# Kernel optimization log

Hardware: AMD Instinct MI355X
Metric: run time of the kernel (lower is better)

The kernel has to match this reference:

```python
import jax, jax.numpy as jnp
import numpy as np
from jax.ops import segment_sum, segment_max

N, E, B = 100000, 400000, 2048
F_NODE, F_EDGE, G_DIM = 7, 3, 10
HID, H, C, L, T = 128, 4, 32, 4, 5
EPS = 1e-5
NEG_SLOPE = 0.2

def setup_inputs():
    key = jax.random.key(0)
    ks = iter(jax.random.split(key, 64))
    def nrm(shape, fan_in):
        return jax.random.normal(next(ks), shape, jnp.float32) / np.float32(np.sqrt(fan_in))
    return {
        "x": jax.random.normal(next(ks), (N, F_NODE), jnp.float32),
        "edge_index": jax.random.randint(next(ks), (2, E), 0, N),
        "edge_attr": jax.random.normal(next(ks), (E, F_EDGE), jnp.float32),
        "batch": jnp.sort(jax.random.randint(next(ks), (N,), 0, B)),
        "global_features": jax.random.normal(next(ks), (B, G_DIM), jnp.float32),
        "node_w": nrm((F_NODE, HID), F_NODE), "node_b": jnp.zeros((HID,), jnp.float32),
        "edge_w": nrm((F_EDGE, HID), F_EDGE), "edge_b": jnp.zeros((HID,), jnp.float32),
        "gat_lin_w": nrm((L, HID, H * C), HID),
        "gat_edge_w": nrm((L, HID, H * C), HID),
        "att_src": nrm((L, H, C), C), "att_dst": nrm((L, H, C), C), "att_edge": nrm((L, H, C), C),
        "gat_bias": jnp.zeros((L, H * C), jnp.float32),
        "bn_gamma": jnp.ones((L, HID), jnp.float32), "bn_beta": jnp.zeros((L, HID), jnp.float32),
        "bn_mean": jnp.zeros((L, HID), jnp.float32), "bn_var": jnp.ones((L, HID), jnp.float32),
        "gc_w": nrm((3 * HID, HID), 3 * HID), "gc_b": jnp.zeros((HID,), jnp.float32),
        "gf1_w": nrm((G_DIM, HID // 2), G_DIM), "gf1_b": jnp.zeros((HID // 2,), jnp.float32),
        "gf2_w": nrm((HID // 2, HID // 2), HID // 2), "gf2_b": jnp.zeros((HID // 2,), jnp.float32),
        "p1_w": nrm((HID + HID // 2, HID), HID + HID // 2), "p1_b": jnp.zeros((HID,), jnp.float32),
        "p2_w": nrm((HID, HID // 2), HID), "p2_b": jnp.zeros((HID // 2,), jnp.float32),
        "p3_w": nrm((HID // 2, T), HID // 2), "p3_b": jnp.zeros((T,), jnp.float32),
    }

def _forward(x, edge_attr, global_features,
             node_w, node_b, edge_w, edge_b,
             gat_lin_w, gat_edge_w, att_src, att_dst, att_edge, gat_bias,
             bn_gamma, bn_beta, bn_mean, bn_var,
             gc_w, gc_b, gf1_w, gf1_b, gf2_w, gf2_b,
             p1_w, p1_b, p2_w, p2_b, p3_w, p3_b,
             edge_index, batch):
    n = x.shape[0]
    b = global_features.shape[0]
    src, dst = edge_index[0], edge_index[1]
    loop = jnp.arange(n)

    h = x @ node_w + node_b                       # [N, HID]
    e = edge_attr @ edge_w + edge_b               # [E, HID]

    # PyG add_self_loops with fill_value='mean': self-loop edge feature is the
    # mean of incoming edge features (0 for isolated nodes).
    deg = segment_sum(jnp.ones((src.shape[0],), h.dtype), dst, num_segments=n)
    e_loop = segment_sum(e, dst, num_segments=n) / jnp.maximum(deg, 1.0)[:, None]
    fsrc = jnp.concatenate([src, loop])
    fdst = jnp.concatenate([dst, loop])
    fe = jnp.concatenate([e, e_loop], axis=0)     # [E+N, HID]

    for i in range(L):
        h_res = h
        xh = (h @ gat_lin_w[i]).reshape(n, H, C)
        eh = (fe @ gat_edge_w[i]).reshape(-1, H, C)
        a_s = jnp.einsum('nhc,hc->nh', xh, att_src[i])
        a_d = jnp.einsum('nhc,hc->nh', xh, att_dst[i])
        a_e = jnp.einsum('ehc,hc->eh', eh, att_edge[i])
        alpha = jax.nn.leaky_relu(a_s[fsrc] + a_d[fdst] + a_e, NEG_SLOPE)  # [E+N, H]
        # segment softmax over destination neighborhoods (self loops => nonempty)
        amax = segment_max(alpha, fdst, num_segments=n)
        expa = jnp.exp(alpha - amax[fdst])
        denom = segment_sum(expa, fdst, num_segments=n)
        coef = expa / denom[fdst]
        out = segment_sum(xh[fsrc] * coef[..., None], fdst, num_segments=n)
        out = out.reshape(n, H * C) + gat_bias[i]
        # BatchNorm (eval-mode running stats)
        out = (out - bn_mean[i]) * (bn_gamma[i] / jnp.sqrt(bn_var[i] + EPS)) + bn_beta[i]
        h = jax.nn.relu(out) + h_res

    # multi-pool readout
    cnt = segment_sum(jnp.ones((n,), h.dtype), batch, num_segments=b)
    gsum = segment_sum(h, batch, num_segments=b)
    gmean = gsum / jnp.maximum(cnt, 1.0)[:, None]
    gmax = segment_max(h, batch, num_segments=b)
    gmax = jnp.where(cnt[:, None] > 0, gmax, 0.0)
    graph = jnp.concatenate([gmean, gmax, gsum], axis=1)   # [B, 3*HID]
    graph = jax.nn.relu(graph @ gc_w + gc_b)
    glob = jax.nn.relu(global_features @ gf1_w + gf1_b) @ gf2_w + gf2_b
    comb = jnp.concatenate([graph, glob], axis=1)          # [B, HID + HID//2]
    hid = jax.nn.relu(comb @ p1_w + p1_b)
    hid = jax.nn.relu(hid @ p2_w + p2_b)
    return hid @ p3_w + p3_b                               # [B, T]

def reference(x, edge_index, edge_attr, batch, global_features,
              node_w, node_b, edge_w, edge_b,
              gat_lin_w, gat_edge_w, att_src, att_dst, att_edge, gat_bias,
              bn_gamma, bn_beta, bn_mean, bn_var,
              gc_w, gc_b, gf1_w, gf1_b, gf2_w, gf2_b,
              p1_w, p1_b, p2_w, p2_b, p3_w, p3_b):
    return _forward(x, edge_attr, global_features,
                    node_w, node_b, edge_w, edge_b,
                    gat_lin_w, gat_edge_w, att_src, att_dst, att_edge, gat_bias,
                    bn_gamma, bn_beta, bn_mean, bn_var,
                    gc_w, gc_b, gf1_w, gf1_b, gf2_w, gf2_b,
                    p1_w, p1_b, p2_w, p2_b, p3_w, p3_b,
                    edge_index, batch)
```

## Files before the change

kernel.cpp:

```cpp
#include <hip/hip_runtime.h>

#define N_NODES 100000
#define N_EDGES 400000
#define N_GRAPHS 2048
#define HID 128
#define NLAYER 4
#define TOUT 5
#define EPSV 1e-5f
#define SLOPE 0.2f
#define NB 98
#define GEMM_BLOCKS 782

typedef float v4f __attribute__((ext_vector_type(4)));
typedef __bf16 v8bf __attribute__((ext_vector_type(8)));

static __device__ __forceinline__ unsigned short f2bf_bits(float f){
  unsigned u = __builtin_bit_cast(unsigned, f);
  unsigned r = u + 0x7fffu + ((u >> 16) & 1u);
  return (unsigned short)(r >> 16);
}
static __device__ __forceinline__ float bfbits2f(unsigned short s){
  unsigned u = ((unsigned)s) << 16;
  return __builtin_bit_cast(float, u);
}
static __device__ __forceinline__ float bflo(unsigned u){
  return __builtin_bit_cast(float, u << 16);
}
static __device__ __forceinline__ float bfhi(unsigned u){
  return __builtin_bit_cast(float, u & 0xffff0000u);
}
static __device__ __forceinline__ float lrelu(float v){
  return v>0.f ? v : SLOPE*v;
}


__global__ void k_setup(const float* __restrict__ gat_edge_w, const float* __restrict__ att_edge,
                        const float* __restrict__ edge_w, const float* __restrict__ edge_b,
                        const float* __restrict__ gat_bias, const float* __restrict__ gamma,
                        const float* __restrict__ beta, const float* __restrict__ mean,
                        const float* __restrict__ var, const float* __restrict__ gat_lin_w,
                        const float* __restrict__ att_src, const float* __restrict__ att_dst,
                        const float* __restrict__ x, const float* __restrict__ nw,
                        const float* __restrict__ nb, unsigned* __restrict__ h16,
                        float* __restrict__ mebuf, float* __restrict__ bnA, float* __restrict__ bnS,
                        unsigned short* __restrict__ whiE, unsigned short* __restrict__ wloE,
                        unsigned short* __restrict__ whi,
                        int* __restrict__ deg, int* __restrict__ fill){
  int bid = blockIdx.x, t = threadIdx.x;
  if(bid < 16){
    int wv = t>>6, lane = t&63;
    int o = bid*4 + wv;
    int li = (o<48)? (o&15) : (o-48);
    int f = o>>4;
    int l = li>>2, hh = li&3;
    int c = lane&31, kk = lane>>5;
    float at_c = att_edge[l*128 + hh*32 + c];
    float acc = 0.f;
    #pragma unroll 8
    for(int t2=0; t2<64; ++t2){
      int k = kk*64 + t2;
      float wk = (o<48)? edge_w[f*128+k] : edge_b[k];
      acc += wk * gat_edge_w[l*16384 + k*128 + hh*32 + c];
    }
    acc *= at_c;
    acc += __shfl_xor(acc,1); acc += __shfl_xor(acc,2); acc += __shfl_xor(acc,4);
    acc += __shfl_xor(acc,8); acc += __shfl_xor(acc,16); acc += __shfl_xor(acc,32);
    if(lane==0) mebuf[o] = acc;
  } else if(bid == 16){
    for(int i=t; i<NLAYER*HID; i+=256){
      int l_ = i>>7, pos = i&127, lane = pos>>2, j = pos&3;
      int ch = ((lane>>3)<<5) + ((lane&7)<<1) + ((j&1)<<4) + (j>>1);
      int src = l_*128 + ch;
      float A = gamma[src]*rsqrtf(var[src]+EPSV);
      bnA[i] = A;
      bnS[i] = (gat_bias[src]-mean[src])*A + beta[src];
    }
  } else if(bid <= 1040){
    int wave = t>>6, lane = t&63;
    int i = (bid-17)*8 + wave*2 + (lane>>5);
    int l_ = i>>11, rest = i&2047, kp = rest>>4, col = rest&15;
    int sub = lane&31;
    float val = 0.f;
    if(col < 8){
      int h_ = col&3, isdst = col>>2;
      int ch = ((kp>>5)<<5) + ((kp&1)<<4) + ((kp&31)>>1);
      const float* at = (isdst? att_dst : att_src);
      val = gat_lin_w[l_*16384 + ch*128 + h_*32 + sub] * at[l_*128 + h_*32 + sub];
    }
    val += __shfl_xor(val,1); val += __shfl_xor(val,2); val += __shfl_xor(val,4);
    val += __shfl_xor(val,8); val += __shfl_xor(val,16);
    if(sub == 0){
      unsigned short hi = f2bf_bits(val);
      unsigned short lo = f2bf_bits(val - bfbits2f(hi));
      int kb=kp>>5, quad=(kp>>3)&3, jj=kp&7, lane2=quad*16+col;
      int dst = ((l_*4+kb)*64 + lane2)*8 + jj;
      whiE[dst]=hi; wloE[dst]=lo;
    }
  } else if(bid <= 1296){
    int tg = (bid-1041)*256 + t;
    int base = tg>>9, off = tg&511;
    int l = base>>5, kb=(base>>3)&3, cg=base&7;
    int lane = off>>3, j = off&7;
    int quad = lane>>4, r = lane&15;
    int kp = kb*32 + quad*8 + j;
    int k = ((kp>>5)<<5) | ((kp&1)<<4) | ((kp&31)>>1);
    whi[tg] = f2bf_bits(gat_lin_w[l*16384 + k*128 + cg*16 + r]);
  } else if(bid <= 1687){
    int tg = (bid-1297)*256 + t;
    if(tg < N_NODES){ deg[tg]=0; fill[tg]=0; }
  } else {
    int node = (bid-1688)*4 + (t>>6);
    int c = t&63;
    int ch = ((c>>4)<<5) + (c&15);
    float a0 = nb[ch], a1 = nb[ch+16];
    #pragma unroll
    for(int f=0; f<7; ++f){
      float xv = x[node*7+f];
      a0 += xv*nw[f*HID+ch];
      a1 += xv*nw[f*HID+ch+16];
    }
    unsigned p = (unsigned)f2bf_bits(a0) | ((unsigned)f2bf_bits(a1)<<16);
    h16[(size_t)node*64 + c] = p;
  }
}

__global__ void k_deg(const int* __restrict__ ei, int* __restrict__ deg){
  int e = blockIdx.x*256 + threadIdx.x;
  if(e < N_EDGES) atomicAdd(&deg[ei[N_EDGES+e]], 1);
}

__global__ void k_scan1(const int* __restrict__ deg, int* __restrict__ part){
  __shared__ int s[256];
  int t=threadIdx.x; int base = blockIdx.x*1024 + t*4;
  int sum=0;
  #pragma unroll
  for(int j=0;j<4;++j){ int i=base+j; sum += (i<N_NODES)? deg[i]:0; }
  s[t]=sum; __syncthreads();
  for(int off=128; off>0; off>>=1){ if(t<off) s[t]+=s[t+off]; __syncthreads(); }
  if(t==0) part[blockIdx.x]=s[0];
}
__global__ void k_scan3(const int* __restrict__ deg, const int* __restrict__ part,
                        int* __restrict__ rowptr){
  __shared__ int s[256];
  int t=threadIdx.x, b=blockIdx.x;
  int g = 0, tot = 0;
  for(int i=0;i<NB;++i){ int v = part[i]; g += (i<b)? v : 0; tot += v; }
  if(b==0 && t==0) rowptr[N_NODES]=tot;
  int base = b*1024 + t*4;
  int v[4]; int sum=0; int pre[4];
  #pragma unroll
  for(int j=0;j<4;++j){ int i=base+j; v[j]=(i<N_NODES)?deg[i]:0; pre[j]=sum; sum+=v[j]; }
  s[t]=sum; __syncthreads();
  for(int off=1; off<256; off<<=1){
    int xv = (t>=off)? s[t-off]:0; __syncthreads();
    s[t]+=xv; __syncthreads();
  }
  int toff = (t>0)? s[t-1]:0;
  #pragma unroll
  for(int j=0;j<4;++j){ int i=base+j; if(i<N_NODES) rowptr[i]=g+toff+pre[j]; }
}

__global__ void k_gemm(const unsigned short* __restrict__ h16,
                       const unsigned short* __restrict__ whi,
                       const unsigned short* __restrict__ whiE,
                       const unsigned short* __restrict__ wloE,
                       unsigned* __restrict__ xhb, float* __restrict__ as_, float* __restrict__ ad_,
                       const int* __restrict__ ei, const float* __restrict__ ea,
                       const int* __restrict__ rowptr, int* __restrict__ fill,
                       int* __restrict__ csr_src, float* __restrict__ ea_csr){
  if(blockIdx.x >= GEMM_BLOCKS){
    int e = (blockIdx.x - GEMM_BLOCKS)*256 + threadIdx.x;
    if(e < N_EDGES){
      int dst = ei[N_EDGES+e];
      int pos = rowptr[dst] + atomicAdd(&fill[dst],1);
      csr_src[pos] = ei[e];
      v4f q = {ea[e*3], ea[e*3+1], ea[e*3+2], 0.f};
      ((v4f*)ea_csr)[pos] = q;
    }
    return;
  }
  __shared__ unsigned sxh[4][2][16*68];
  int wave = threadIdx.x>>6, lane = threadIdx.x&63;
  int base = blockIdx.x*128;
  int q = lane>>4, r = lane&15;
  int r0[2];
  r0[0] = base + wave*16;
  r0[1] = base + 64 + wave*16;
  if(r0[0] > N_NODES-16) r0[0] = N_NODES-16;
  if(r0[1] > N_NODES-16) r0[1] = N_NODES-16;
  v8bf av[2][4];
  #pragma unroll
  for(int tt=0;tt<2;++tt){
    const unsigned short* hrow = h16 + (size_t)(r0[tt] + r)*HID;
    #pragma unroll
    for(int kb=0;kb<4;++kb)
      av[tt][kb] = *(const v8bf*)(hrow + kb*32 + q*8);
  }
  v4f acc[2][8];
  #pragma unroll
  for(int cg=0;cg<8;++cg){
    v4f a0 = {0.f,0.f,0.f,0.f}, a1 = {0.f,0.f,0.f,0.f};
    #pragma unroll
    for(int kb=0;kb<4;++kb){
      v8bf bhi = *(const v8bf*)(whi + ((kb*8+cg)*64 + lane)*8);
      a0 = __builtin_amdgcn_mfma_f32_16x16x32_bf16(av[0][kb], bhi, a0, 0,0,0);
      a1 = __builtin_amdgcn_mfma_f32_16x16x32_bf16(av[1][kb], bhi, a1, 0,0,0);
    }
    acc[0][cg]=a0; acc[1][cg]=a1;
  }
  v4f acc8[2] = {{0.f,0.f,0.f,0.f},{0.f,0.f,0.f,0.f}};
  #pragma unroll
  for(int kb=0;kb<4;++kb){
    v8bf bhi = *(const v8bf*)(whiE + (kb*64 + lane)*8);
    v8bf blo = *(const v8bf*)(wloE + (kb*64 + lane)*8);
    #pragma unroll
    for(int tt=0;tt<2;++tt){
      acc8[tt] = __builtin_amdgcn_mfma_f32_16x16x32_bf16(av[tt][kb], blo, acc8[tt], 0,0,0);
      acc8[tt] = __builtin_amdgcn_mfma_f32_16x16x32_bf16(av[tt][kb], bhi, acc8[tt], 0,0,0);
    }
  }
  #pragma unroll
  for(int tt=0;tt<2;++tt){
    #pragma unroll
    for(int m=0;m<4;++m){
      #pragma unroll
      for(int reg=0;reg<4;++reg){
        unsigned pack = (unsigned)f2bf_bits(acc[tt][2*m][reg]) | ((unsigned)f2bf_bits(acc[tt][2*m+1][reg])<<16);
        sxh[wave][tt][(q*4+reg)*68 + m*16 + r] = pack;
      }
    }
  }
  __syncthreads();
  {
    int rr = lane>>4, c4 = lane&15;
    #pragma unroll
    for(int tt=0;tt<2;++tt){
      #pragma unroll
      for(int rg=0; rg<4; ++rg){
        int i = rg*4 + rr;
        uint4 v = *(const uint4*)&sxh[wave][tt][i*68 + c4*4];
        *(uint4*)(xhb + (size_t)(r0[tt] + i)*64 + c4*4) = v;
      }
    }
  }
  #pragma unroll
  for(int tt=0;tt<2;++tt){
    if(r < 4){
      #pragma unroll
      for(int reg=0;reg<4;++reg)
        as_[(size_t)(r0[tt] + q*4 + reg)*4 + r] = acc8[tt][reg];
    } else if(r < 8){
      #pragma unroll
      for(int reg=0;reg<4;++reg)
        ad_[(size_t)(r0[tt] + q*4 + reg)*4 + (r-4)] = acc8[tt][reg];
    }
  }
}

__global__ void k_aggr(const unsigned* __restrict__ xhb, const float* __restrict__ as_,
    const float* __restrict__ ad_, const float* __restrict__ ea_csr,
    const float* __restrict__ mebuf,
    const int* __restrict__ rowptr, const int* __restrict__ csr_src,
    const float* __restrict__ bnA_l, const float* __restrict__ bnS_l,
    unsigned* __restrict__ h16, int layer){
  __shared__ float lds_coef[8][16*4];
  __shared__ int   lds_src[8][16];
  int hw = threadIdx.x>>5, lh = threadIdx.x&31;
  int lane = threadIdx.x&63;
  int node = blockIdx.x*8 + hw;
  if(node >= N_NODES) return;
  int s = rowptr[node], e = rowptr[node+1];
  int deg = e - s;
  int hh2 = lh>>3;
  const uint2* xrow = (const uint2*)xhb;
  float a0,a1,a2,a3;

  if(deg <= 16){
    int eidx = lh>>2, h = lh&3;
    int li = layer*4+h;
    float mec0=mebuf[li], mec1=mebuf[16+li], mec2=mebuf[32+li], meb=mebuf[48+li];
    float ad_h = ad_[node*4+h];
    int j0 = eidx;
    float t0 = 0.f, g0 = 0.f;
    int s0 = node;
    bool v0 = (j0 < deg);
    if(v0){
      s0 = csr_src[s+j0];
      v4f qq = ((const v4f*)ea_csr)[s+j0];
      t0 = qq.x*mec0 + qq.y*mec1 + qq.z*mec2;
      g0 = lrelu(as_[s0*4+h] + ad_h + t0 + meb);
    }
    float ts, ds, inv;
    if(deg <= 8){
      ts = t0;
      ts += __shfl_xor(ts,4); ts += __shfl_xor(ts,8); ts += __shfl_xor(ts,16);
      float lt = (deg>0) ? ts/(float)deg + meb : 0.f;
      float al = lrelu(as_[node*4+h] + ad_h + lt);
      float e0 = v0 ? __expf(g0-al) : 0.f;
      ds = e0;
      ds += __shfl_xor(ds,4); ds += __shfl_xor(ds,8); ds += __shfl_xor(ds,16);
      inv = 1.f/(ds+1.f);
      if(h==0) lds_src[hw][j0] = s0;
      lds_coef[hw][j0*4+h] = e0*inv;
    } else {
      int j1 = 8+eidx;
      float t1 = 0.f, g1 = 0.f;
      int s1 = node;
      bool v1 = (j1 < deg);
      if(v1){
        s1 = csr_src[s+j1];
        v4f qq = ((const v4f*)ea_csr)[s+j1];
        t1 = qq.x*mec0 + qq.y*mec1 + qq.z*mec2;
        g1 = lrelu(as_[s1*4+h] + ad_h + t1 + meb);
      }
      ts = t0+t1;
      ts += __shfl_xor(ts,4); ts += __shfl_xor(ts,8); ts += __shfl_xor(ts,16);
      float lt = ts/(float)deg + meb;
      float al = lrelu(as_[node*4+h] + ad_h + lt);
      float e0 = v0 ? __expf(g0-al) : 0.f;
      float e1 = v1 ? __expf(g1-al) : 0.f;
      ds = e0+e1;
      ds += __shfl_xor(ds,4); ds += __shfl_xor(ds,8); ds += __shfl_xor(ds,16);
      inv = 1.f/(ds+1.f);
      if(h==0){ lds_src[hw][j0]=s0; lds_src[hw][j1]=s1; }
      lds_coef[hw][j0*4+h] = e0*inv;
      lds_coef[hw][j1*4+h] = e1*inv;
    }
    float cs4 = __shfl(inv, (lane&32) | hh2);
    uint2 su = xrow[(size_t)node*32 + lh];
    int pdeg = (deg+1)&~1;
    a0=a1=a2=a3=0.f;
    for(int j=0;j<pdeg;j+=2){
      float ca = lds_coef[hw][j*4+hh2];
      float cb = lds_coef[hw][(j+1)*4+hh2];
      int sa = lds_src[hw][j], sb = lds_src[hw][j+1];
      uint2 ua = xrow[(size_t)sa*32+lh];
      uint2 ub = xrow[(size_t)sb*32+lh];
      a0 += ca*bflo(ua.x) + cb*bflo(ub.x);
      a1 += ca*bfhi(ua.x) + cb*bfhi(ub.x);
      a2 += ca*bflo(ua.y) + cb*bflo(ub.y);
      a3 += ca*bfhi(ua.y) + cb*bfhi(ub.y);
    }
    a0 += cs4*bflo(su.x); a1 += cs4*bfhi(su.x);
    a2 += cs4*bflo(su.y); a3 += cs4*bfhi(su.y);
  } else {
    int li = layer*4+hh2;
    float mec0=mebuf[li], mec1=mebuf[16+li], mec2=mebuf[32+li], meb=mebuf[48+li];
    float adv = ad_[node*4+hh2];
    float ts = 0.f;
    for(int j=s;j<e;++j){
      v4f qq = ((const v4f*)ea_csr)[j];
      ts += qq.x*mec0 + qq.y*mec1 + qq.z*mec2;
    }
    float al = lrelu(as_[node*4+hh2] + adv + ts/(float)deg + meb);
    float m = al, d = 1.f;
    uint2 su = xrow[(size_t)node*32 + lh];
    float c0=bflo(su.x),c1=bfhi(su.x),c2=bflo(su.y),c3=bfhi(su.y);
    for(int j=s;j<e;++j){
      int sr = csr_src[j];
      v4f qq = ((const v4f*)ea_csr)[j];
      float b = lrelu(as_[sr*4+hh2] + adv + qq.x*mec0+qq.y*mec1+qq.z*mec2+meb);
      uint2 uv = xrow[(size_t)sr*32 + lh];
      float nm = fmaxf(m,b);
      float sc = __expf(m-nm), eb = __expf(b-nm);
      d = d*sc + eb;
      c0 = c0*sc + eb*bflo(uv.x); c1 = c1*sc + eb*bfhi(uv.x);
      c2 = c2*sc + eb*bflo(uv.y); c3 = c3*sc + eb*bfhi(uv.y);
      m = nm;
    }
    float inv2 = 1.f/d;
    a0=c0*inv2; a1=c1*inv2; a2=c2*inv2; a3=c3*inv2;
  }

  {
    const v4f* A4 = (const v4f*)bnA_l;
    const v4f* S4 = (const v4f*)bnS_l;
    v4f A = A4[lh], S = S4[lh];
    uint2 hr = ((const uint2*)h16)[(size_t)node*32 + lh];
    float o0 = fmaxf(a0*A.x+S.x, 0.f) + bflo(hr.x);
    float o1 = fmaxf(a1*A.y+S.y, 0.f) + bfhi(hr.x);
    float o2 = fmaxf(a2*A.z+S.z, 0.f) + bflo(hr.y);
    float o3 = fmaxf(a3*A.w+S.w, 0.f) + bfhi(hr.y);
    uint2 p;
    p.x = (unsigned)f2bf_bits(o0) | ((unsigned)f2bf_bits(o1)<<16);
    p.y = (unsigned)f2bf_bits(o2) | ((unsigned)f2bf_bits(o3)<<16);
    ((uint2*)h16)[(size_t)node*32 + lh] = p;
  }
}

__global__ void k_tail(const unsigned* __restrict__ h16, const int* __restrict__ batch,
   const float* __restrict__ gf,
   const float* __restrict__ gc_w, const float* __restrict__ gc_b,
   const float* __restrict__ gf1_w, const float* __restrict__ gf1_b,
   const float* __restrict__ gf2_w, const float* __restrict__ gf2_b,
   const float* __restrict__ p1_w, const float* __restrict__ p1_b,
   const float* __restrict__ p2_w, const float* __restrict__ p2_b,
   const float* __restrict__ p3_w, const float* __restrict__ p3_b,
   float* __restrict__ out){
  __shared__ float sg[384];
  __shared__ int sb[2];
  __shared__ float comb[192];
  __shared__ float hid1[64];
  __shared__ float r1[128];
  __shared__ float r2[64];
  int g = blockIdx.x, t = threadIdx.x;
  if(t < 2){
    int target = g + t;
    int lo=0, hi=N_NODES;
    while(lo<hi){ int mid=(lo+hi)>>1; if(batch[mid] < target) lo=mid+1; else hi=mid; }
    sb[t]=lo;
  }
  __syncthreads();
  {
    int s = sb[0], e = sb[1];
    int u = ((t>>5)<<4) + (t&15);
    int hiflag = (t>>4)&1;
    float sum=0.f, mx=-3.4e38f;
    for(int i=s;i<e;++i){
      unsigned uv = h16[(size_t)i*64 + u];
      float v = hiflag ? bfhi(uv) : bflo(uv);
      sum+=v; mx=fmaxf(mx,v);
    }
    int cnt = e-s;
    float meanv = sum / (float)(cnt>1?cnt:1);
    if(cnt==0) mx=0.f;
    sg[t] = meanv;
    sg[128+t] = mx;
    sg[256+t] = sum;
  }
  if(t<64){
    float a = gf1_b[t];
    #pragma unroll
    for(int i=0;i<10;++i) a += gf[g*10+i]*gf1_w[i*64+t];
    hid1[t] = fmaxf(a,0.f);
  }
  __syncthreads();
  if(t<64){
    float a = gf2_b[t];
    for(int k=0;k<64;++k) a += hid1[k]*gf2_w[k*64+t];
    comb[128+t] = a;
  }
  {
    float a = gc_b[t];
    for(int k=0;k<384;++k) a += sg[k]*gc_w[k*128+t];
    comb[t] = fmaxf(a,0.f);
  }
  __syncthreads();
  {
    float a = p1_b[t];
    for(int k=0;k<192;++k) a += comb[k]*p1_w[k*128+t];
    r1[t] = fmaxf(a,0.f);
  }
  __syncthreads();
  if(t<64){
    float a = p2_b[t];
    for(int k=0;k<128;++k) a += r1[k]*p2_w[k*64+t];
    r2[t] = fmaxf(a,0.f);
  }
  __syncthreads();
  if(t<TOUT){
    float a = p3_b[t];
    for(int k=0;k<64;++k) a += r2[k]*p3_w[k*TOUT+t];
    out[g*TOUT+t] = a;
  }
}

extern "C" void kernel_launch(void* const* d_in, const int* in_sizes, int n_in,
                              void* d_out, int out_size, void* d_ws, size_t ws_size,
                              hipStream_t stream){
  (void)in_sizes; (void)n_in; (void)out_size; (void)ws_size;
  const float* x        = (const float*)d_in[0];
  const int*   ei       = (const int*)d_in[1];
  const float* ea       = (const float*)d_in[2];
  const int*   batch    = (const int*)d_in[3];
  const float* gfin     = (const float*)d_in[4];
  const float* node_w   = (const float*)d_in[5];
  const float* node_b   = (const float*)d_in[6];
  const float* edge_w   = (const float*)d_in[7];
  const float* edge_b   = (const float*)d_in[8];
  const float* gat_lin_w  = (const float*)d_in[9];
  const float* gat_edge_w = (const float*)d_in[10];
  const float* att_src  = (const float*)d_in[11];
  const float* att_dst  = (const float*)d_in[12];
  const float* att_edge = (const float*)d_in[13];
  const float* gat_bias = (const float*)d_in[14];
  const float* bn_gamma = (const float*)d_in[15];
  const float* bn_beta  = (const float*)d_in[16];
  const float* bn_mean  = (const float*)d_in[17];
  const float* bn_var   = (const float*)d_in[18];
  const float* gc_w = (const float*)d_in[19];
  const float* gc_b = (const float*)d_in[20];
  const float* gf1_w = (const float*)d_in[21];
  const float* gf1_b = (const float*)d_in[22];
  const float* gf2_w = (const float*)d_in[23];
  const float* gf2_b = (const float*)d_in[24];
  const float* p1_w = (const float*)d_in[25];
  const float* p1_b = (const float*)d_in[26];
  const float* p2_w = (const float*)d_in[27];
  const float* p2_b = (const float*)d_in[28];
  const float* p3_w = (const float*)d_in[29];
  const float* p3_b = (const float*)d_in[30];
  float* out = (float*)d_out;

  char* w = (char*)d_ws;
  size_t o = 0;
  auto carve = [&](size_t bytes)->char*{
    char* p = w + o; o += (bytes + 255) & ~(size_t)255; return p;
  };
  unsigned* xhb = (unsigned*)carve((size_t)N_NODES*64*4);
  unsigned* h16 = (unsigned*)carve((size_t)N_NODES*64*4);
  float* ea_csr = (float*)carve((size_t)N_EDGES*4*4);
  float* as_    = (float*)carve((size_t)N_NODES*4*4);
  float* ad_    = (float*)carve((size_t)N_NODES*4*4);
  int* deg      = (int*)carve((size_t)N_NODES*4);
  int* rowptr   = (int*)carve((size_t)(N_NODES+1)*4);
  int* fill     = (int*)carve((size_t)N_NODES*4);
  int* csr_src  = (int*)carve((size_t)N_EDGES*4);
  int* part     = (int*)carve(1024*4);
  float* mebuf  = (float*)carve(64*4);
  float* bnA    = (float*)carve((size_t)NLAYER*HID*4);
  float* bnS    = (float*)carve((size_t)NLAYER*HID*4);
  unsigned short* whi = (unsigned short*)carve(65536*2);
  unsigned short* whiE = (unsigned short*)carve(8192*2);
  unsigned short* wloE = (unsigned short*)carve(8192*2);

  k_setup<<<1688 + N_NODES/4, 256, 0, stream>>>(gat_edge_w, att_edge, edge_w, edge_b,
        gat_bias, bn_gamma, bn_beta, bn_mean, bn_var,
        gat_lin_w, att_src, att_dst, x, node_w, node_b, h16,
        mebuf, bnA, bnS, whiE, wloE, whi, deg, fill);
  k_deg<<<(N_EDGES+255)/256, 256, 0, stream>>>(ei, deg);
  k_scan1<<<NB,256,0,stream>>>(deg, part);
  k_scan3<<<NB,256,0,stream>>>(deg, part, rowptr);

  for(int l=0;l<NLAYER;++l){
    int gb = (l==0) ? GEMM_BLOCKS + (N_EDGES+255)/256 : GEMM_BLOCKS;
    k_gemm<<<gb,256,0,stream>>>((const unsigned short*)h16,
        whi + l*16384, whiE + l*2048, wloE + l*2048,
        xhb, as_, ad_, ei, ea, rowptr, fill, csr_src, ea_csr);
    k_aggr<<<(N_NODES+7)/8,256,0,stream>>>(xhb, as_, ad_, ea_csr, mebuf,
        rowptr, csr_src, bnA + l*128, bnS + l*128, h16, l);
  }

  k_tail<<<N_GRAPHS,128,0,stream>>>(h16, batch, gfin, gc_w, gc_b, gf1_w, gf1_b,
        gf2_w, gf2_b, p1_w, p1_b, p2_w, p2_b, p3_w, p3_b, out);
}
```

Baseline: 437.8 us.

## Batch eight graphs per block in tail MLP to reuse weights

The tail kernel now processes eight graphs per 256-thread block instead of one per 128-thread block. Pooling is parallelised across row groups with vectorised uint2 loads and a shared-memory reduction. Each MLP weight load is reused across eight graphs, with split-K partial sums combined in shared memory. This cuts redundant weight reads and raises parallelism in pooling, at the cost of far fewer blocks, more shared memory and more syncs.

```diff
diff --git a/kernel.cpp b/kernel.cpp
--- a/kernel.cpp
+++ b/kernel.cpp
@@ -397,71 +397,184 @@
    const float* __restrict__ p2_w, const float* __restrict__ p2_b,
    const float* __restrict__ p3_w, const float* __restrict__ p3_b,
    float* __restrict__ out){
-  __shared__ float sg[384];
-  __shared__ int sb[2];
-  __shared__ float comb[192];
-  __shared__ float hid1[64];
-  __shared__ float r1[128];
-  __shared__ float r2[64];
-  int g = blockIdx.x, t = threadIdx.x;
-  if(t < 2){
-    int target = g + t;
+  __shared__ float sgtT[384*12];
+  __shared__ v4f   redA[256];
+  __shared__ v4f   redB[256];
+  __shared__ float hid1s[8*64];
+  __shared__ float combT[192*12];
+  __shared__ float partialb[8*128];
+  __shared__ float r1T[128*12];
+  __shared__ float ppb[3*8*64];
+  __shared__ float r2T[64*12];
+  __shared__ int   sbv[9];
+
+  int t = threadIdx.x;
+  int g0 = blockIdx.x*8;
+
+  if(t < 9){
+    int target = g0 + t;
     int lo=0, hi=N_NODES;
     while(lo<hi){ int mid=(lo+hi)>>1; if(batch[mid] < target) lo=mid+1; else hi=mid; }
-    sb[t]=lo;
+    sbv[t]=lo;
   }
   __syncthreads();
-  {
-    int s = sb[0], e = sb[1];
-    int u = ((t>>5)<<4) + (t&15);
-    int hiflag = (t>>4)&1;
-    float sum=0.f, mx=-3.4e38f;
-    for(int i=s;i<e;++i){
-      unsigned uv = h16[(size_t)i*64 + u];
-      float v = hiflag ? bfhi(uv) : bflo(uv);
-      sum+=v; mx=fmaxf(mx,v);
-    }
-    int cnt = e-s;
-    float meanv = sum / (float)(cnt>1?cnt:1);
-    if(cnt==0) mx=0.f;
-    sg[t] = meanv;
-    sg[128+t] = mx;
-    sg[256+t] = sum;
-  }
-  if(t<64){
-    float a = gf1_b[t];
-    #pragma unroll
-    for(int i=0;i<10;++i) a += gf[g*10+i]*gf1_w[i*64+t];
-    hid1[t] = fmaxf(a,0.f);
+
+  {
+    int w2 = t&31;
+    int j8 = t>>5;
+    const uint2* xr = (const uint2*)h16;
+    for(int g=0; g<8; ++g){
+      int s=sbv[g], e=sbv[g+1];
+      float sl0=0.f,sh0=0.f,sl1=0.f,sh1=0.f;
+      float ml0=-3.4e38f, mh0=-3.4e38f, ml1=-3.4e38f, mh1=-3.4e38f;
+      for(int i=s+j8; i<e; i+=8){
+        uint2 v = xr[(size_t)i*32 + w2];
+        float a=bflo(v.x), b=bfhi(v.x), c=bflo(v.y), d=bfhi(v.y);
+        sl0+=a; sh0+=b; sl1+=c; sh1+=d;
+        ml0=fmaxf(ml0,a); mh0=fmaxf(mh0,b); ml1=fmaxf(ml1,c); mh1=fmaxf(mh1,d);
+      }
+      redA[t] = (v4f){sl0,sh0,sl1,sh1};
+      redB[t] = (v4f){ml0,mh0,ml1,mh1};
+      __syncthreads();
+      if(t < 32){
+        v4f S = redA[t], M = redB[t];
+        #pragma unroll
+        for(int jj=1; jj<8; ++jj){
+          v4f a2 = redA[jj*32+t], b2 = redB[jj*32+t];
+          S.x+=a2.x; S.y+=a2.y; S.z+=a2.z; S.w+=a2.w;
+          M.x=fmaxf(M.x,b2.x); M.y=fmaxf(M.y,b2.y);
+          M.z=fmaxf(M.z,b2.z); M.w=fmaxf(M.w,b2.w);
+        }
+        int cnt = sbv[g+1]-sbv[g];
+        float invc = 1.f/(float)(cnt>1?cnt:1);
+        if(cnt==0){ M.x=0.f; M.y=0.f; M.z=0.f; M.w=0.f; }
+        int bb = w2>>3, rr = (w2&7)*2;
+        int c00 = bb*32+rr, c01=c00+16, c10=c00+1, c11=c00+17;
+        sgtT[c00*12+g]=S.x*invc; sgtT[c01*12+g]=S.y*invc;
+        sgtT[c10*12+g]=S.z*invc; sgtT[c11*12+g]=S.w*invc;
+        sgtT[(128+c00)*12+g]=M.x; sgtT[(128+c01)*12+g]=M.y;
+        sgtT[(128+c10)*12+g]=M.z; sgtT[(128+c11)*12+g]=M.w;
+        sgtT[(256+c00)*12+g]=S.x; sgtT[(256+c01)*12+g]=S.y;
+        sgtT[(256+c10)*12+g]=S.z; sgtT[(256+c11)*12+g]=S.w;
+      }
+      __syncthreads();
+    }
+  }
+
+  {
+    int c=t&63, gg=t>>6;
+    #pragma unroll
+    for(int p=0;p<2;++p){
+      int g = p*4+gg;
+      float a = gf1_b[c];
+      #pragma unroll
+      for(int i=0;i<10;++i) a += gf[(size_t)(g0+g)*10+i]*gf1_w[i*64+c];
+      hid1s[g*64+c] = fmaxf(a,0.f);
+    }
+  }
+
+  int c = t&127, half = t>>7;
+  float acc[8];
+  #pragma unroll
+  for(int g=0;g<8;++g) acc[g]=0.f;
+  {
+    int kb = half*192;
+    for(int kk=0; kk<192; ++kk){
+      int k = kb+kk;
+      float wv = gc_w[k*128+c];
+      v4f s0v = *(const v4f*)&sgtT[k*12];
+      v4f s1v = *(const v4f*)&sgtT[k*12+4];
+      acc[0]+=s0v.x*wv; acc[1]+=s0v.y*wv; acc[2]+=s0v.z*wv; acc[3]+=s0v.w*wv;
+      acc[4]+=s1v.x*wv; acc[5]+=s1v.y*wv; acc[6]+=s1v.z*wv; acc[7]+=s1v.w*wv;
+    }
   }
   __syncthreads();
-  if(t<64){
-    float a = gf2_b[t];
-    for(int k=0;k<64;++k) a += hid1[k]*gf2_w[k*64+t];
-    comb[128+t] = a;
-  }
-  {
-    float a = gc_b[t];
-    for(int k=0;k<384;++k) a += sg[k]*gc_w[k*128+t];
-    comb[t] = fmaxf(a,0.f);
+
+  {
+    int cc=t&63, gg=t>>6;
+    #pragma unroll
+    for(int p=0;p<2;++p){
+      int g = p*4+gg;
+      float a = gf2_b[cc];
+      for(int k=0;k<64;++k) a += hid1s[g*64+k]*gf2_w[k*64+cc];
+      combT[(128+cc)*12+g] = a;
+    }
+  }
+  if(half==1){
+    #pragma unroll
+    for(int g=0;g<8;++g) partialb[g*128+c]=acc[g];
   }
   __syncthreads();
-  {
-    float a = p1_b[t];
-    for(int k=0;k<192;++k) a += comb[k]*p1_w[k*128+t];
-    r1[t] = fmaxf(a,0.f);
+  if(half==0){
+    float bias = gc_b[c];
+    #pragma unroll
+    for(int g=0;g<8;++g)
+      combT[c*12+g] = fmaxf(acc[g]+partialb[g*128+c]+bias, 0.f);
   }
   __syncthreads();
-  if(t<64){
-    float a = p2_b[t];
-    for(int k=0;k<128;++k) a += r1[k]*p2_w[k*64+t];
-    r2[t] = fmaxf(a,0.f);
+
+  float a1[8];
+  #pragma unroll
+  for(int g=0;g<8;++g) a1[g]=0.f;
+  {
+    int kb = half*96;
+    for(int kk=0; kk<96; ++kk){
+      int k = kb+kk;
+      float wv = p1_w[k*128+c];
+      v4f s0v = *(const v4f*)&combT[k*12];
+      v4f s1v = *(const v4f*)&combT[k*12+4];
+      a1[0]+=s0v.x*wv; a1[1]+=s0v.y*wv; a1[2]+=s0v.z*wv; a1[3]+=s0v.w*wv;
+      a1[4]+=s1v.x*wv; a1[5]+=s1v.y*wv; a1[6]+=s1v.z*wv; a1[7]+=s1v.w*wv;
+    }
+  }
+  if(half==1){
+    #pragma unroll
+    for(int g=0;g<8;++g) partialb[g*128+c]=a1[g];
   }
   __syncthreads();
-  if(t<TOUT){
-    float a = p3_b[t];
-    for(int k=0;k<64;++k) a += r2[k]*p3_w[k*TOUT+t];
-    out[g*TOUT+t] = a;
+  if(half==0){
+    float b1 = p1_b[c];
+    #pragma unroll
+    for(int g=0;g<8;++g)
+      r1T[c*12+g] = fmaxf(a1[g]+partialb[g*128+c]+b1, 0.f);
+  }
+  __syncthreads();
+
+  {
+    int c2=t&63, qd=t>>6;
+    float a2[8];
+    #pragma unroll
+    for(int g=0;g<8;++g) a2[g]=0.f;
+    int kb = qd*32;
+    for(int kk=0; kk<32; ++kk){
+      int k = kb+kk;
+      float wv = p2_w[k*64+c2];
+      v4f s0v = *(const v4f*)&r1T[k*12];
+      v4f s1v = *(const v4f*)&r1T[k*12+4];
+      a2[0]+=s0v.x*wv; a2[1]+=s0v.y*wv; a2[2]+=s0v.z*wv; a2[3]+=s0v.w*wv;
+      a2[4]+=s1v.x*wv; a2[5]+=s1v.y*wv; a2[6]+=s1v.z*wv; a2[7]+=s1v.w*wv;
+    }
+    if(qd>0){
+      #pragma unroll
+      for(int g=0;g<8;++g) ppb[((qd-1)*8+g)*64+c2]=a2[g];
+    }
+    __syncthreads();
+    if(qd==0){
+      float b2 = p2_b[c2];
+      #pragma unroll
+      for(int g=0;g<8;++g){
+        float v = a2[g] + ppb[g*64+c2] + ppb[(8+g)*64+c2] + ppb[(16+g)*64+c2] + b2;
+        r2T[c2*12+g] = fmaxf(v,0.f);
+      }
+    }
+    __syncthreads();
+  }
+
+  if(t < 40){
+    int g = t/5, o = t%5;
+    float a = p3_b[o];
+    for(int k=0;k<64;++k) a += r2T[k*12+g]*p3_w[k*TOUT+o];
+    out[(size_t)(g0+g)*TOUT+o] = a;
   }
 }
 
@@ -541,6 +654,6 @@
         rowptr, csr_src, bnA + l*128, bnS + l*128, h16, l);
   }
 
-  k_tail<<<N_GRAPHS,128,0,stream>>>(h16, batch, gfin, gc_w, gc_b, gf1_w, gf1_b,
+  k_tail<<<N_GRAPHS/8,256,0,stream>>>(h16, batch, gfin, gc_w, gc_b, gf1_w, gf1_b,
         gf2_w, gf2_b, p1_w, p1_b, p2_w, p2_b, p3_w, p3_b, out);
 }
```

New measurement: 432.8 us. Within noise of the previous version (-1.1%).
